# Kernel optimization log

Measured on AMD Instinct MI355X. Metric: run time of the kernel, lower is better.

The kernel has to match this reference:

```python
import jax, jax.numpy as jnp
import numpy as np

WIN, HOP, OFF, K = 32000, 4000, 8000, 256
SEG = 2 * OFF


def setup_inputs() -> dict:
    key = jax.random.key(0)
    T = 40_000_000  # ~41.6 minutes @ 16 kHz
    inputs = jax.random.normal(key, (1, 1, T), dtype=jnp.float32)
    return {"inputs": inputs}


def reference(inputs):
    a = jnp.abs(inputs[0, 0])  # (T,)
    T = a.shape[0]
    n_win = (T - WIN) // HOP + 1
    blocks = a[: (T // HOP) * HOP].reshape(-1, HOP).sum(axis=1)  # (T//HOP,)
    bc = jnp.concatenate([jnp.zeros(1, blocks.dtype), jnp.cumsum(blocks)])
    r = WIN // HOP
    means = (bc[r : r + n_win] - bc[:n_win]) / WIN  # sliding-window means
    # top-K loudest windows, chunk centers sorted by position
    _, idx = jax.lax.top_k(means, K)
    centers = jnp.sort(idx * HOP + WIN // 2)  # (K,)
    # torchaudio linear Fade with fade_in_len=fade_out_len=SEG: mask = t*(1-t)
    t = jnp.linspace(0.0, 1.0, SEG, dtype=inputs.dtype)
    mask = t * (1.0 - t)
    def grab(c):
        return jax.lax.dynamic_slice(inputs, (0, 0, c - OFF), (1, 1, SEG))
    segs = jax.vmap(grab)(centers)  # (K,1,1,SEG)
    segs = segs * mask
    # concat segments along time axis
    return jnp.transpose(segs, (1, 2, 0, 3)).reshape(1, 1, K * SEG)
```

## Files before the change

kernel.cpp:

```cpp
#include <hip/hip_runtime.h>
#include <math.h>


#define T_LEN  40000000
#define HOP    4000
#define NBLK   10000
#define NWIN   9993
#define KSEL   256
#define SEG    16000
#define OFF    8000

__global__ __launch_bounds__(256) void k_blocksums(const float* __restrict__ in,
                                                   float* __restrict__ blocks) {
    const int half = threadIdx.x >> 5;
    const int j    = threadIdx.x & 31;
    const int row  = blockIdx.x * 8 + half;
    const float* p = in + (size_t)row * 4000 + j;
    float acc = 0.0f;
    #pragma unroll 5
    for (int i = 0; i < 125; ++i) acc += fabsf(p[i * 32]);
    acc += __shfl_xor(acc, 16);
    acc += __shfl_xor(acc, 8);
    acc += __shfl_xor(acc, 4);
    acc += __shfl_xor(acc, 2);
    acc += __shfl_xor(acc, 1);
    if (j == 0) blocks[row] = acc;
}

__global__ __launch_bounds__(1024) void k_select(const float* __restrict__ blocks,
                                                 unsigned* __restrict__ um,
                                                 int* __restrict__ sel) {
    __shared__ float sb[NBLK];
    __shared__ float s0[625];
    __shared__ float w1[640];
    __shared__ float s1[40];
    __shared__ float w2[48];
    __shared__ float s2[3];
    __shared__ float p3[3];
    __shared__ float p2s[40];
    __shared__ float p1s[625];
    __shared__ unsigned hist[256];
    __shared__ unsigned sc[1024];
    __shared__ unsigned sc2[1024];
    __shared__ unsigned s_pfx, s_k;
    const int tid = threadIdx.x;

    for (int i = tid; i < NBLK; i += 1024) sb[i] = blocks[i];
    __syncthreads();

    if (tid < 625) {
        const int base = tid * 16;
        float s = sb[base];
        #pragma unroll
        for (int j = 1; j < 16; ++j) { s += sb[base + j]; sb[base + j] = s; }
        s0[tid] = s;
    }
    __syncthreads();
    if (tid < 40) {
        const int base = tid * 16;
        const int cnt  = (tid == 39) ? 1 : 16;
        float s = s0[base];
        w1[base] = s;
        for (int j = 1; j < cnt; ++j) { s += s0[base + j]; w1[base + j] = s; }
        s1[tid] = s;
    }
    __syncthreads();
    if (tid < 3) {
        const int base = tid * 16;
        const int cnt  = (tid == 2) ? 8 : 16;
        float s = s1[base];
        w2[base] = s;
        for (int j = 1; j < cnt; ++j) { s += s1[base + j]; w2[base + j] = s; }
        s2[tid] = s;
    }
    __syncthreads();
    if (tid == 0) {
        p3[0] = 0.0f;
        p3[1] = s2[0];
        p3[2] = s2[0] + s2[1];
        s_pfx = 0u; s_k = KSEL;
    }
    __syncthreads();
    if (tid < 40) p2s[tid] = p3[tid >> 4] + w2[tid];
    __syncthreads();
    if (tid < 625) {
        const int c = tid >> 4;
        const float P2 = (c == 0) ? 0.0f : p2s[c - 1];
        p1s[tid] = P2 + w1[tid];
    }
    __syncthreads();
    for (int i = tid; i < NBLK; i += 1024) {
        const int b = i >> 4;
        const float P1 = (b == 0) ? 0.0f : p1s[b - 1];
        sb[i] = P1 + sb[i];
    }
    __syncthreads();
    for (int i = tid; i < NWIN; i += 1024) {
        const float lo = (i == 0) ? 0.0f : sb[i - 1];
        const float m = (sb[i + 7] - lo) / 32000.0f;
        um[i] = __float_as_uint(m);
    }
    __syncthreads();

    for (int pass = 0; pass < 4; ++pass) {
        const int shift = 24 - pass * 8;
        if (tid < 256) hist[tid] = 0u;
        __syncthreads();
        const unsigned pfx = s_pfx;
        const unsigned kcur = s_k;
        for (int i = tid; i < NWIN; i += 1024) {
            unsigned u = um[i];
            bool cand = (pass == 0) || ((u >> (shift + 8)) == pfx);
            if (cand) atomicAdd(&hist[(u >> shift) & 255u], 1u);
        }
        __syncthreads();
        if (tid < 256) {
            unsigned suf = 0;
            for (int jj = tid; jj < 256; ++jj) suf += hist[jj];
            unsigned above = suf - hist[tid];
            if (suf >= kcur && above < kcur) {
                s_pfx = (pfx << 8) | (unsigned)tid;
                s_k = kcur - above;
            }
        }
        __syncthreads();
    }
    const unsigned C   = s_pfx;
    const unsigned keq = s_k;

    const int lo = tid * 10;
    const int hi = (lo + 10 < NWIN) ? lo + 10 : NWIN;
    unsigned ceq = 0, cgt = 0;
    for (int i = lo; i < hi; ++i) {
        unsigned u = um[i];
        cgt += (u > C) ? 1u : 0u;
        ceq += (u == C) ? 1u : 0u;
    }
    sc[tid] = ceq; sc2[tid] = cgt;
    __syncthreads();
    for (int ofs = 1; ofs < 1024; ofs <<= 1) {
        unsigned av = 0, bv = 0;
        if (tid >= ofs) { av = sc[tid - ofs]; bv = sc2[tid - ofs]; }
        __syncthreads();
        if (tid >= ofs) { sc[tid] += av; sc2[tid] += bv; }
        __syncthreads();
    }
    unsigned e = sc[tid]  - ceq;
    unsigned g = sc2[tid] - cgt;
    for (int i = lo; i < hi; ++i) {
        unsigned u = um[i];
        if (u > C) {
            unsigned esel = (e < keq) ? e : keq;
            sel[g + esel] = i;
            ++g;
        } else if (u == C) {
            if (e < keq) sel[g + e] = i;
            ++e;
        }
    }
}

__global__ __launch_bounds__(256) void k_gather(const float* __restrict__ in,
                                                const int* __restrict__ sel,
                                                float* __restrict__ out) {
    const int b = blockIdx.x;
    const int s = b >> 2;
    const int part = b & 3;
    const int w = sel[s];
    const float4* ip = (const float4*)(in + (size_t)w * HOP + OFF);
    float4* op = (float4*)(out + (size_t)s * SEG);
    const double st = 1.0 / 15999.0;
    const int v0 = part * 1000;
    for (int v = v0 + threadIdx.x; v < v0 + 1000; v += 256) {
        float4 x = ip[v];
        int jj = v * 4;
        float t0 = (float)(jj * st);
        float t1 = (float)((jj + 1) * st);
        float t2 = (float)((jj + 2) * st);
        float t3 = (jj + 3 == 15999) ? 1.0f : (float)((jj + 3) * st);
        x.x *= t0 * (1.0f - t0);
        x.y *= t1 * (1.0f - t1);
        x.z *= t2 * (1.0f - t2);
        x.w *= t3 * (1.0f - t3);
        op[v] = x;
    }
}

extern "C" void kernel_launch(void* const* d_in, const int* in_sizes, int n_in,
                              void* d_out, int out_size, void* d_ws, size_t ws_size,
                              hipStream_t stream) {
    (void)in_sizes; (void)n_in; (void)out_size; (void)ws_size;
    const float* in = (const float*)d_in[0];
    float* out = (float*)d_out;
    char* ws = (char*)d_ws;
    float*    blocks = (float*)ws;
    unsigned* um     = (unsigned*)(ws + 40960);
    int*      sel    = (int*)(ws + 81920);
    k_blocksums<<<dim3(NBLK / 8), dim3(256), 0, stream>>>(in, blocks);
    k_select<<<dim3(1), dim3(1024), 0, stream>>>(blocks, um, sel);
    k_gather<<<dim3(KSEL * 4), dim3(256), 0, stream>>>(in, sel, out);
}
```

Before: 268.9 us.

## Vectorize block-sum loads and keep window means in registers for radix select

The block-sum kernel now loads float4 with 8 threads per row and 16 rows per 128-thread block, replacing scalar loads with 32 threads per row. The select kernel keeps each thread's 10 window means in registers instead of round-tripping through a global array. It uses per-wave histograms to cut LDS atomic contention, plus shuffle-based wave scans for the suffix sums and the final compaction scan, replacing serial loops and many-barrier scans. Packing two 16-bit counters into one word relies on counts staying below 65536.

After: 257.2 us. 1.05x faster.

```diff
diff --git a/kernel.cpp b/kernel.cpp
--- a/kernel.cpp
+++ b/kernel.cpp
@@ -10,17 +10,19 @@
 #define SEG    16000
 #define OFF    8000
 
-__global__ __launch_bounds__(256) void k_blocksums(const float* __restrict__ in,
+__global__ __launch_bounds__(128) void k_blocksums(const float* __restrict__ in,
                                                    float* __restrict__ blocks) {
-    const int half = threadIdx.x >> 5;
-    const int j    = threadIdx.x & 31;
-    const int row  = blockIdx.x * 8 + half;
-    const float* p = in + (size_t)row * 4000 + j;
-    float acc = 0.0f;
+    const int g   = threadIdx.x >> 3;
+    const int j   = threadIdx.x & 7;
+    const int row = blockIdx.x * 16 + g;
+    const float4* p = (const float4*)(in + (size_t)row * HOP) + j;
+    float ax = 0.0f, ay = 0.0f, az = 0.0f, aw = 0.0f;
     #pragma unroll 5
-    for (int i = 0; i < 125; ++i) acc += fabsf(p[i * 32]);
-    acc += __shfl_xor(acc, 16);
-    acc += __shfl_xor(acc, 8);
+    for (int i = 0; i < 125; ++i) {
+        const float4 x = p[(size_t)i * 8];
+        ax += fabsf(x.x); ay += fabsf(x.y); az += fabsf(x.z); aw += fabsf(x.w);
+    }
+    float acc = (ax + ay) + (az + aw);
     acc += __shfl_xor(acc, 4);
     acc += __shfl_xor(acc, 2);
     acc += __shfl_xor(acc, 1);
@@ -28,7 +30,6 @@
 }
 
 __global__ __launch_bounds__(1024) void k_select(const float* __restrict__ blocks,
-                                                 unsigned* __restrict__ um,
                                                  int* __restrict__ sel) {
     __shared__ float sb[NBLK];
     __shared__ float s0[625];
@@ -39,11 +40,14 @@
     __shared__ float p3[3];
     __shared__ float p2s[40];
     __shared__ float p1s[625];
+    __shared__ unsigned whist[16][257];
     __shared__ unsigned hist[256];
-    __shared__ unsigned sc[1024];
-    __shared__ unsigned sc2[1024];
+    __shared__ unsigned rw[4];
+    __shared__ unsigned wsum[16];
     __shared__ unsigned s_pfx, s_k;
-    const int tid = threadIdx.x;
+    const int tid  = threadIdx.x;
+    const int lane = tid & 63;
+    const int wid  = tid >> 6;
 
     for (int i = tid; i < NBLK; i += 1024) sb[i] = blocks[i];
     __syncthreads();
@@ -58,19 +62,19 @@
     __syncthreads();
     if (tid < 40) {
         const int base = tid * 16;
-        const int cnt  = (tid == 39) ? 1 : 16;
+        const int cnt1 = (tid == 39) ? 1 : 16;
         float s = s0[base];
         w1[base] = s;
-        for (int j = 1; j < cnt; ++j) { s += s0[base + j]; w1[base + j] = s; }
+        for (int j = 1; j < cnt1; ++j) { s += s0[base + j]; w1[base + j] = s; }
         s1[tid] = s;
     }
     __syncthreads();
     if (tid < 3) {
         const int base = tid * 16;
-        const int cnt  = (tid == 2) ? 8 : 16;
+        const int cnt2 = (tid == 2) ? 8 : 16;
         float s = s1[base];
         w2[base] = s;
-        for (int j = 1; j < cnt; ++j) { s += s1[base + j]; w2[base + j] = s; }
+        for (int j = 1; j < cnt2; ++j) { s += s1[base + j]; w2[base + j] = s; }
         s2[tid] = s;
     }
     __syncthreads();
@@ -95,32 +99,62 @@
         sb[i] = P1 + sb[i];
     }
     __syncthreads();
-    for (int i = tid; i < NWIN; i += 1024) {
-        const float lo = (i == 0) ? 0.0f : sb[i - 1];
-        const float m = (sb[i + 7] - lo) / 32000.0f;
-        um[i] = __float_as_uint(m);
-    }
-    __syncthreads();
+
+    const int lo  = tid * 10;
+    const int cnt = (lo < NWIN) ? ((lo + 10 <= NWIN) ? 10 : NWIN - lo) : 0;
+    unsigned uv[10];
+    #pragma unroll
+    for (int r = 0; r < 10; ++r) {
+        if (r < cnt) {
+            const int i = lo + r;
+            const float lof = (i == 0) ? 0.0f : sb[i - 1];
+            const float m = (sb[i + 7] - lof) / 32000.0f;
+            uv[r] = __float_as_uint(m);
+        }
+    }
 
     for (int pass = 0; pass < 4; ++pass) {
         const int shift = 24 - pass * 8;
-        if (tid < 256) hist[tid] = 0u;
-        __syncthreads();
-        const unsigned pfx = s_pfx;
+        for (int i = tid; i < 16 * 257; i += 1024) ((unsigned*)whist)[i] = 0u;
+        __syncthreads();
+        const unsigned pfx  = s_pfx;
         const unsigned kcur = s_k;
-        for (int i = tid; i < NWIN; i += 1024) {
-            unsigned u = um[i];
-            bool cand = (pass == 0) || ((u >> (shift + 8)) == pfx);
-            if (cand) atomicAdd(&hist[(u >> shift) & 255u], 1u);
+        #pragma unroll
+        for (int r = 0; r < 10; ++r) {
+            if (r < cnt) {
+                const unsigned u = uv[r];
+                const bool cand = (pass == 0) || ((u >> (shift + 8)) == pfx);
+                if (cand) atomicAdd(&whist[wid][(u >> shift) & 255u], 1u);
+            }
         }
         __syncthreads();
         if (tid < 256) {
-            unsigned suf = 0;
-            for (int jj = tid; jj < 256; ++jj) suf += hist[jj];
-            unsigned above = suf - hist[tid];
+            unsigned s = 0;
+            #pragma unroll
+            for (int w = 0; w < 16; ++w) s += whist[w][tid];
+            hist[tid] = s;
+        }
+        __syncthreads();
+        unsigned inc = 0, h = 0;
+        if (tid < 256) {
+            h = hist[255 - tid];
+            inc = h;
+            #pragma unroll
+            for (int o = 1; o < 64; o <<= 1) {
+                const unsigned n = __shfl_up(inc, o);
+                if (lane >= o) inc += n;
+            }
+            if (lane == 63) rw[tid >> 6] = inc;
+        }
+        __syncthreads();
+        if (tid < 256) {
+            unsigned add = 0;
+            for (int k = 0; k < (tid >> 6); ++k) add += rw[k];
+            const unsigned suf   = inc + add;
+            const unsigned above = suf - h;
             if (suf >= kcur && above < kcur) {
-                s_pfx = (pfx << 8) | (unsigned)tid;
-                s_k = kcur - above;
+                s_pfx = (pfx << 8) | (unsigned)(255 - tid);
+                s_k   = kcur - above;
             }
         }
         __syncthreads();
@@ -128,34 +162,41 @@
     const unsigned C   = s_pfx;
     const unsigned keq = s_k;
 
-    const int lo = tid * 10;
-    const int hi = (lo + 10 < NWIN) ? lo + 10 : NWIN;
     unsigned ceq = 0, cgt = 0;
-    for (int i = lo; i < hi; ++i) {
-        unsigned u = um[i];
-        cgt += (u > C) ? 1u : 0u;
-        ceq += (u == C) ? 1u : 0u;
-    }
-    sc[tid] = ceq; sc2[tid] = cgt;
-    __syncthreads();
-    for (int ofs = 1; ofs < 1024; ofs <<= 1) {
-        unsigned av = 0, bv = 0;
-        if (tid >= ofs) { av = sc[tid - ofs]; bv = sc2[tid - ofs]; }
-        __syncthreads();
-        if (tid >= ofs) { sc[tid] += av; sc2[tid] += bv; }
-        __syncthreads();
-    }
-    unsigned e = sc[tid]  - ceq;
-    unsigned g = sc2[tid] - cgt;
-    for (int i = lo; i < hi; ++i) {
-        unsigned u = um[i];
-        if (u > C) {
-            unsigned esel = (e < keq) ? e : keq;
-            sel[g + esel] = i;
-            ++g;
-        } else if (u == C) {
-            if (e < keq) sel[g + e] = i;
-            ++e;
+    #pragma unroll
+    for (int r = 0; r < 10; ++r) {
+        if (r < cnt) {
+            const unsigned u = uv[r];
+            cgt += (u > C)  ? 1u : 0u;
+            ceq += (u == C) ? 1u : 0u;
+        }
+    }
+    const unsigned pack = ceq | (cgt << 16);
+    unsigned incp = pack;
+    #pragma unroll
+    for (int o = 1; o < 64; o <<= 1) {
+        const unsigned n = __shfl_up(incp, o);
+        if (lane >= o) incp += n;
+    }
+    if (lane == 63) wsum[wid] = incp;
+    __syncthreads();
+    unsigned woffv = 0;
+    for (int w = 0; w < wid; ++w) woffv += wsum[w];
+    const unsigned ex = incp - pack + woffv;
+    unsigned e = ex & 0xFFFFu;
+    unsigned g = ex >> 16;
+    #pragma unroll
+    for (int r = 0; r < 10; ++r) {
+        if (r < cnt) {
+            const unsigned u = uv[r];
+            if (u > C) {
+                const unsigned esel = (e < keq) ? e : keq;
+                sel[g + esel] = lo + r;
+                ++g;
+            } else if (u == C) {
+                if (e < keq) sel[g + e] = lo + r;
+                ++e;
+            }
         }
     }
 }
@@ -193,10 +234,9 @@
     const float* in = (const float*)d_in[0];
     float* out = (float*)d_out;
     char* ws = (char*)d_ws;
-    float*    blocks = (float*)ws;
-    unsigned* um     = (unsigned*)(ws + 40960);
-    int*      sel    = (int*)(ws + 81920);
-    k_blocksums<<<dim3(NBLK / 8), dim3(256), 0, stream>>>(in, blocks);
-    k_select<<<dim3(1), dim3(1024), 0, stream>>>(blocks, um, sel);
+    float* blocks = (float*)ws;
+    int*   sel    = (int*)(ws + 40960);
+    k_blocksums<<<dim3(625), dim3(128), 0, stream>>>(in, blocks);
+    k_select<<<dim3(1), dim3(1024), 0, stream>>>(blocks, sel);
     k_gather<<<dim3(KSEL * 4), dim3(256), 0, stream>>>(in, sel, out);
 }
```
